# Kernel tuning notes

Hardware: AMD Instinct MI355X
Metric: run time of the kernel (lower is better)

Reference implementation:

```python
import jax, jax.numpy as jnp
from jax import lax
import numpy as np
import math

# --- static config (matches init_kwargs) ---
B, L, C_IN = 64, 1024, 16
D, H, D_FF = 256, 8, 1024
HS, E_LAYERS, OUT = 256, 2, 1
MA, FACTOR = 25, 3
TOP_K = int(FACTOR * math.log(L))  # 20


def _ln(x, g, b, eps=1e-5):
    m = x.mean(-1, keepdims=True)
    v = ((x - m) ** 2).mean(-1, keepdims=True)
    return (x - m) / jnp.sqrt(v + eps) * g + b


def _series_decomp(x, k):
    # x: [B, L, C]; replicate-pad then moving average (AvgPool1d stride 1)
    pad = (k - 1) // 2
    front = jnp.repeat(x[:, :1, :], pad, axis=1)
    end = jnp.repeat(x[:, -1:, :], pad, axis=1)
    xp = jnp.concatenate([front, x, end], axis=1)  # [B, L+k-1, C]
    cs = jnp.cumsum(xp, axis=1)
    cs = jnp.concatenate([jnp.zeros_like(cs[:, :1]), cs], axis=1)
    mm = (cs[:, k:] - cs[:, :-k]) / k  # [B, L, C]
    return x - mm, mm


def _autocorrelation(q, k, v):
    # q,k,v: [B, L, H, E] -> eval-mode Autoformer AutoCorrelation
    Bq, Lq, Hq, Eq = q.shape
    qf = jnp.fft.rfft(q.transpose(0, 2, 3, 1), axis=-1)  # [B,H,E,F]
    kf = jnp.fft.rfft(k.transpose(0, 2, 3, 1), axis=-1)
    corr = jnp.fft.irfft(qf * jnp.conj(kf), n=Lq, axis=-1)  # [B,H,E,L]
    mean_value = corr.mean(axis=(1, 2))  # [B, L]
    weights, delay = lax.top_k(mean_value, TOP_K)  # [B, K]
    tmp_corr = jax.nn.softmax(weights, axis=-1)
    vals = v.transpose(0, 2, 3, 1)  # [B,H,E,L]
    init = jnp.arange(Lq)

    def step(acc, dw):
        d, w = dw  # d: [B] int, w: [B] float
        idx = (init[None, :] + d[:, None]) % Lq  # circular delayed gather == roll
        pat = jnp.take_along_axis(vals, idx[:, None, None, :], axis=-1)
        return acc + pat * w[:, None, None, None], None

    agg, _ = lax.scan(step, jnp.zeros_like(vals), (delay.T, tmp_corr.T))
    return agg.transpose(0, 3, 1, 2)  # [B, L, H, E]


def _forward(x_enc, conv1_w, conv1_b, conv2_w, conv2_b, cnn_ln_g, cnn_ln_b,
             proj_w, proj_b, proj_ln_g, proj_ln_b,
             Wq, bq, Wk, bk, Wv, bv, Wo, bo, Wff1, Wff2,
             rp1_w, rp1_b, rp_ln_g, rp_ln_b, rp2_w, rp2_b):
    Bb = x_enc.shape[0]
    dn = ('NCH', 'OIH', 'NCH')
    # CNN frontend (dropout = identity in eval)
    h = lax.conv_general_dilated(x_enc.transpose(0, 2, 1), conv1_w, (1,), [(1, 1)],
                                 dimension_numbers=dn) + conv1_b[None, :, None]
    h = jax.nn.relu(h)
    h = lax.conv_general_dilated(h, conv2_w, (1,), [(1, 1)],
                                 dimension_numbers=dn) + conv2_b[None, :, None]
    h = jax.nn.relu(h)
    enc = _ln(h.transpose(0, 2, 1), cnn_ln_g, cnn_ln_b)  # [B, L, D]

    pooled_parts = []
    for i in range(E_LAYERS):
        q = (enc @ Wq[i] + bq[i]).reshape(Bb, L, H, D // H)
        k = (enc @ Wk[i] + bk[i]).reshape(Bb, L, H, D // H)
        v = (enc @ Wv[i] + bv[i]).reshape(Bb, L, H, D // H)
        ac = _autocorrelation(q, k, v).reshape(Bb, L, D)
        new_x = ac @ Wo[i] + bo[i]
        x = enc + new_x
        x, _ = _series_decomp(x, MA)
        y = jax.nn.gelu(jnp.einsum('bld,fd->blf', x, Wff1[i]), approximate=False)
        y = jnp.einsum('blf,df->bld', y, Wff2[i])
        enc, _ = _series_decomp(x + y, MA)
        pooled_parts.append(enc[:, -1, :])

    pooled = jnp.concatenate(pooled_parts, axis=-1)  # [B, e_layers*D]
    input_embed = _ln(jax.nn.relu(x_enc.reshape(Bb, -1) @ proj_w + proj_b),
                      proj_ln_g, proj_ln_b)  # [B, HS]
    final = jnp.concatenate([pooled, input_embed], axis=-1)
    o = jax.nn.relu(final @ rp1_w + rp1_b)
    o = _ln(o, rp_ln_g, rp_ln_b)
    o = o @ rp2_w + rp2_b  # [B, 1]
    return o.squeeze(-1)


def setup_inputs() -> dict:
    key = jax.random.key(0)
    ks = iter(jax.random.split(key, 32))

    def nrm(shape, s=0.02):
        return jax.random.normal(next(ks), shape, jnp.float32) * s

    inp = {
        'x_enc': jax.random.normal(next(ks), (B, L, C_IN), jnp.float32),
        'conv1_w': nrm((D, C_IN, 3), 0.1), 'conv1_b': jnp.zeros((D,), jnp.float32),
        'conv2_w': nrm((D, D, 3), 0.05), 'conv2_b': jnp.zeros((D,), jnp.float32),
        'cnn_ln_g': jnp.ones((D,), jnp.float32), 'cnn_ln_b': jnp.zeros((D,), jnp.float32),
        'proj_w': nrm((L * C_IN, HS)), 'proj_b': jnp.zeros((HS,), jnp.float32),
        'proj_ln_g': jnp.ones((HS,), jnp.float32), 'proj_ln_b': jnp.zeros((HS,), jnp.float32),
        'Wq': nrm((E_LAYERS, D, D)), 'bq': jnp.zeros((E_LAYERS, D), jnp.float32),
        'Wk': nrm((E_LAYERS, D, D)), 'bk': jnp.zeros((E_LAYERS, D), jnp.float32),
        'Wv': nrm((E_LAYERS, D, D)), 'bv': jnp.zeros((E_LAYERS, D), jnp.float32),
        'Wo': nrm((E_LAYERS, D, D)), 'bo': jnp.zeros((E_LAYERS, D), jnp.float32),
        'Wff1': nrm((E_LAYERS, D_FF, D)),
        'Wff2': nrm((E_LAYERS, D, D_FF)),
        'rp1_w': nrm((E_LAYERS * D + HS, HS)), 'rp1_b': jnp.zeros((HS,), jnp.float32),
        'rp_ln_g': jnp.ones((HS,), jnp.float32), 'rp_ln_b': jnp.zeros((HS,), jnp.float32),
        'rp2_w': nrm((HS, OUT)), 'rp2_b': jnp.zeros((OUT,), jnp.float32),
    }
    return inp


def reference(x_enc, conv1_w, conv1_b, conv2_w, conv2_b, cnn_ln_g, cnn_ln_b,
              proj_w, proj_b, proj_ln_g, proj_ln_b,
              Wq, bq, Wk, bk, Wv, bv, Wo, bo, Wff1, Wff2,
              rp1_w, rp1_b, rp_ln_g, rp_ln_b, rp2_w, rp2_b):
    return _forward(x_enc, conv1_w, conv1_b, conv2_w, conv2_b, cnn_ln_g, cnn_ln_b,
                    proj_w, proj_b, proj_ln_g, proj_ln_b,
                    Wq, bq, Wk, bk, Wv, bv, Wo, bo, Wff1, Wff2,
                    rp1_w, rp1_b, rp_ln_g, rp_ln_b, rp2_w, rp2_b)
```

## Files before the change

kernel.cpp:

```cpp
#include <hip/hip_runtime.h>
#include <math.h>

#define FLAG_ACC     1
#define FLAG_RELU    2
#define FLAG_GELU    4
#define FLAG_ABF16   8
#define FLAG_OBF16  16
#define FLAG_RESB16 32

typedef __attribute__((ext_vector_type(8))) short short8;
typedef __attribute__((ext_vector_type(4))) short short4v;
typedef __attribute__((ext_vector_type(4))) float f32x4;

__device__ __forceinline__ short f2bf(float f) {
  unsigned u = __builtin_bit_cast(unsigned, f);
  unsigned r = u + 0x7fffu + ((u >> 16) & 1u);
  return (short)(r >> 16);
}
__device__ __forceinline__ float bf2f(short s) {
  unsigned u = ((unsigned)(unsigned short)s) << 16;
  return __builtin_bit_cast(float, u);
}
__device__ __forceinline__ void load_lds16(const void* g, void* lds) {
  __builtin_amdgcn_global_load_lds(
      (const __attribute__((address_space(1))) void*)g,
      (__attribute__((address_space(3))) void*)lds, 16, 0, 0);
}

__global__ __launch_bounds__(256) void gemm_f32(
    const float* __restrict__ A, const float* __restrict__ B, float* __restrict__ C,
    int M, int N, int K, int a_shift,
    const float* __restrict__ bias, const float* __restrict__ residual, int flags)
{
  __shared__ float As[16][65];
  __shared__ float Bs[16][64];
  const int tid = threadIdx.x;
  const int tx = tid & 15, ty = tid >> 4;
  const int row0 = blockIdx.y * 64;
  const int col0 = blockIdx.x * 64;
  int kbeg = 0, kend = K;
  if ((int)gridDim.z > 1) {
    int kchunk = ((K + (int)gridDim.z - 1) / (int)gridDim.z + 15) & ~15;
    kbeg = (int)blockIdx.z * kchunk;
    kend = min(K, kbeg + kchunk);
  }
  float acc[4][4] = {};
  const int a_m = tid >> 2;
  const int a_k = (tid & 3) << 2;
  const int b_n = (tid & 15) << 2;
  const int b_k = tid >> 4;
  for (int k0 = kbeg; k0 < kend; k0 += 16) {
    int srow = row0 + a_m + a_shift;
    float4 av = make_float4(0.f, 0.f, 0.f, 0.f);
    if (srow >= 0 && srow < M)
      av = *reinterpret_cast<const float4*>(A + (long long)srow * K + (k0 + a_k));
    As[a_k + 0][a_m] = av.x; As[a_k + 1][a_m] = av.y;
    As[a_k + 2][a_m] = av.z; As[a_k + 3][a_m] = av.w;
    float4 bv = make_float4(0.f, 0.f, 0.f, 0.f);
    int brow = k0 + b_k;
    if (brow < K)
      bv = *reinterpret_cast<const float4*>(B + (long long)brow * N + (col0 + b_n));
    Bs[b_k][b_n + 0] = bv.x; Bs[b_k][b_n + 1] = bv.y;
    Bs[b_k][b_n + 2] = bv.z; Bs[b_k][b_n + 3] = bv.w;
    __syncthreads();
#pragma unroll
    for (int kk = 0; kk < 16; kk++) {
      float ar[4], br[4];
#pragma unroll
      for (int i = 0; i < 4; i++) ar[i] = As[kk][ty * 4 + i];
#pragma unroll
      for (int j = 0; j < 4; j++) br[j] = Bs[kk][tx * 4 + j];
#pragma unroll
      for (int i = 0; i < 4; i++)
#pragma unroll
        for (int j = 0; j < 4; j++)
          acc[i][j] += ar[i] * br[j];
    }
    __syncthreads();
  }
  if ((int)gridDim.z > 1) {
#pragma unroll
    for (int i = 0; i < 4; i++) {
      int r = row0 + ty * 4 + i; if (r >= M) continue;
#pragma unroll
      for (int j = 0; j < 4; j++) {
        int c = col0 + tx * 4 + j; if (c >= N) continue;
        atomicAdd(&C[(long long)r * N + c], acc[i][j]);
      }
    }
    return;
  }
#pragma unroll
  for (int i = 0; i < 4; i++) {
    int r = row0 + ty * 4 + i; if (r >= M) continue;
#pragma unroll
    for (int j = 0; j < 4; j++) {
      int c = col0 + tx * 4 + j; if (c >= N) continue;
      float v = acc[i][j];
      if (bias)     v += bias[c];
      if (residual) v += residual[(long long)r * N + c];
      if (flags & FLAG_ACC)  v += C[(long long)r * N + c];
      if (flags & FLAG_RELU) v = fmaxf(v, 0.f);
      if (flags & FLAG_GELU) v = 0.5f * v * (1.f + erff(v * 0.70710678118654752f));
      C[(long long)r * N + c] = v;
    }
  }
}

__global__ __launch_bounds__(256) void gemm_bf16_bt(
    const void* __restrict__ Av, const short* __restrict__ Btb, void* __restrict__ Cv,
    const float* __restrict__ residual, const float* __restrict__ bias,
    int M, int N, int K, int lda, int flags, int tapped)
{
  __shared__ __align__(16) short Asl[8192];
  __shared__ __align__(16) short Bsl[8192];
  const int tid = threadIdx.x;
  const int row0 = blockIdx.x * 128;
  const int col0 = blockIdx.y * 128;
  const int lane = tid & 63;
  const int wave = tid >> 6;
  const int wm = (wave >> 1) * 64;
  const int wn = (wave & 1) * 64;
  const int fm = lane & 15;
  const int k8c = lane >> 4;
  const int mr = tid >> 1;
  const int mkc = (tid & 1) * 4;
  const int msw = mr & 7;
  const bool a_dma = (flags & FLAG_ABF16) && !tapped;

  f32x4 acc[4][4] = {};
  for (int k0 = 0; k0 < K; k0 += 64) {
    __syncthreads();
#pragma unroll
    for (int u = 0; u < 4; u++) {
      int p = (wave * 4 + u) * 64 + lane;
      int r = p >> 3;
      int kc = (p & 7) ^ (r & 7);
      load_lds16(Btb + (long long)(col0 + r) * K + k0 + kc * 8,
                 (char*)Bsl + (wave * 4 + u) * 1024);
    }
    if (a_dma) {
      const short* Ab = (const short*)Av;
#pragma unroll
      for (int u = 0; u < 4; u++) {
        int p = (wave * 4 + u) * 64 + lane;
        int r = p >> 3;
        int kc = (p & 7) ^ (r & 7);
        load_lds16(Ab + (long long)(row0 + r) * lda + k0 + kc * 8,
                   (char*)Asl + (wave * 4 + u) * 1024);
      }
    } else {
      int arow = row0 + mr + (tapped ? (k0 >> 8) - 1 : 0);
      int acol = tapped ? (k0 & 255) : k0;
      bool ok = (arow >= 0 && arow < M);
      if (flags & FLAG_ABF16) {
        const short* ga = (const short*)Av + (long long)arow * lda + acol + mkc * 8;
        short8 z;
#pragma unroll
        for (int u = 0; u < 8; u++) z[u] = 0;
#pragma unroll
        for (int j = 0; j < 4; j++) {
          short8 v = ok ? *(const short8*)(ga + j * 8) : z;
          *(short8*)&Asl[(mr * 8 + ((mkc + j) ^ msw)) * 8] = v;
        }
      } else {
        const float* ga = (const float*)Av + (long long)arow * lda + acol + mkc * 8;
#pragma unroll
        for (int j = 0; j < 4; j++) {
          float4 f0 = make_float4(0.f,0.f,0.f,0.f), f1 = f0;
          if (ok) { f0 = *(const float4*)(ga + j * 8); f1 = *(const float4*)(ga + j * 8 + 4); }
          short8 v;
          v[0]=f2bf(f0.x); v[1]=f2bf(f0.y); v[2]=f2bf(f0.z); v[3]=f2bf(f0.w);
          v[4]=f2bf(f1.x); v[5]=f2bf(f1.y); v[6]=f2bf(f1.z); v[7]=f2bf(f1.w);
          *(short8*)&Asl[(mr * 8 + ((mkc + j) ^ msw)) * 8] = v;
        }
      }
    }
    __syncthreads();
#pragma unroll
    for (int kk8 = 0; kk8 < 8; kk8 += 4) {
      short8 af[4], bf[4];
#pragma unroll
      for (int i = 0; i < 4; i++) {
        int r = wm + i * 16 + fm;
        af[i] = *(short8*)&Asl[(r * 8 + ((kk8 + k8c) ^ (r & 7))) * 8];
      }
#pragma unroll
      for (int j = 0; j < 4; j++) {
        int r = wn + j * 16 + fm;
        bf[j] = *(short8*)&Bsl[(r * 8 + ((kk8 + k8c) ^ (r & 7))) * 8];
      }
#pragma unroll
      for (int i = 0; i < 4; i++)
#pragma unroll
        for (int j = 0; j < 4; j++)
          acc[i][j] = __builtin_amdgcn_mfma_f32_16x16x32_bf16(af[i], bf[j], acc[i][j], 0, 0, 0);
    }
  }
#pragma unroll
  for (int i = 0; i < 4; i++) {
    const int mbase = row0 + wm + i * 16 + (lane >> 4) * 4;
#pragma unroll
    for (int j = 0; j < 4; j++) {
      const int n = col0 + wn + j * 16 + fm;
      const float bs = bias ? bias[n] : 0.f;
#pragma unroll
      for (int r = 0; r < 4; r++) {
        long long idx = (long long)(mbase + r) * N + n;
        float v = acc[i][j][r] + bs;
        if (residual) {
          if (flags & FLAG_RESB16) v += bf2f(((const short*)residual)[idx]);
          else                     v += residual[idx];
        }
        if (flags & FLAG_ACC)  v += ((const float*)Cv)[idx];
        if (flags & FLAG_RELU) v = fmaxf(v, 0.f);
        if (flags & FLAG_GELU) v = 0.5f * v * (1.f + erff(v * 0.70710678118654752f));
        if (flags & FLAG_OBF16) ((short*)Cv)[idx] = f2bf(v);
        else                    ((float*)Cv)[idx] = v;
      }
    }
  }
}

__global__ __launch_bounds__(256) void gemm_qk2(
    const short* __restrict__ Ab, const short* __restrict__ Bth,
    const short* __restrict__ Btl,
    short* __restrict__ Ch, short* __restrict__ Cl,
    const float* __restrict__ bias, int M, int N, int K)
{
  __shared__ __align__(16) char smem[24576];
  short* Asl = (short*)smem;
  short* Bhi = (short*)(smem + 8192);
  short* Blo = (short*)(smem + 16384);
  const int tid = threadIdx.x;
  const int row0 = blockIdx.x * 128;
  const int col0 = blockIdx.y * 128;
  const int lane = tid & 63;
  const int wave = tid >> 6;
  const int wm = (wave >> 1) * 64;
  const int wn = (wave & 1) * 64;
  const int fm = lane & 15;
  const int k8c = lane >> 4;

  f32x4 acc[4][4] = {};
  for (int k0 = 0; k0 < K; k0 += 32) {
    __syncthreads();
#pragma unroll
    for (int u = 0; u < 2; u++) {
      int p = (wave + u * 4) * 64 + lane;
      int r = p >> 2;
      int kc = (p & 3) ^ ((r >> 1) & 3);
      long long ao = (long long)(row0 + r) * 256 + k0 + kc * 8;
      long long go = (long long)(col0 + r) * K + k0 + kc * 8;
      int lo = (wave + u * 4) * 1024;
      load_lds16(Ab + ao, (char*)Asl + lo);
      load_lds16(Bth + go, (char*)Bhi + lo);
      load_lds16(Btl + go, (char*)Blo + lo);
    }
    __syncthreads();
    short8 af[4], bh[4], bl[4];
#pragma unroll
    for (int i = 0; i < 4; i++) {
      int r = wm + i * 16 + fm;
      af[i] = *(short8*)&Asl[(r * 4 + (k8c ^ ((r >> 1) & 3))) * 8];
    }
#pragma unroll
    for (int j = 0; j < 4; j++) {
      int r = wn + j * 16 + fm;
      int p = (r * 4 + (k8c ^ ((r >> 1) & 3))) * 8;
      bh[j] = *(short8*)&Bhi[p];
      bl[j] = *(short8*)&Blo[p];
    }
#pragma unroll
    for (int i = 0; i < 4; i++)
#pragma unroll
      for (int j = 0; j < 4; j++) {
        acc[i][j] = __builtin_amdgcn_mfma_f32_16x16x32_bf16(af[i], bh[j], acc[i][j], 0, 0, 0);
        acc[i][j] = __builtin_amdgcn_mfma_f32_16x16x32_bf16(af[i], bl[j], acc[i][j], 0, 0, 0);
      }
  }
#pragma unroll
  for (int i = 0; i < 4; i++) {
    const int mbase = row0 + wm + i * 16 + (lane >> 4) * 4;
#pragma unroll
    for (int j = 0; j < 4; j++) {
      const int n = col0 + wn + j * 16 + fm;
      const float bs = bias ? bias[n] : 0.f;
#pragma unroll
      for (int r = 0; r < 4; r++) {
        long long idx = (long long)(mbase + r) * N + n;
        float v = acc[i][j][r] + bs;
        short h = f2bf(v);
        short l = f2bf(v - bf2f(h));
        Ch[idx] = h; Cl[idx] = l;
      }
    }
  }
}

__global__ __launch_bounds__(256) void corr_mfma3(
    const short* __restrict__ qkh, const short* __restrict__ qkl, float* __restrict__ mv16)
{
  __shared__ __align__(16) char smem[65536];
  short* Ahi = (short*)smem;
  short* Alo = (short*)(smem + 16384);
  short* Bhi = (short*)(smem + 32768);
  short* Blo = (short*)(smem + 49152);
  float* Sf = (float*)smem;

  const int id = blockIdx.x;
  const int b  = (id & 7) + 8 * (id >> 9);
  const int tile = (id >> 3) & 63;
  const int t0 = (tile >> 3) * 128;
  const int s0 = (tile & 7) * 128;
  const int tid = threadIdx.x;
  const int lane = tid & 63;
  const int wave = tid >> 6;
  const int wm = (wave >> 1) * 64;
  const int wn = (wave & 1) * 64;
  const int fm = lane & 15;
  const int k8c = lane >> 4;
  const long long bb = (long long)b * 524288;

  f32x4 acc[4][4] = {};
  for (int k0 = 0; k0 < 256; k0 += 64) {
    __syncthreads();
#pragma unroll
    for (int u = 0; u < 4; u++) {
      int p = (wave * 4 + u) * 64 + lane;
      int r = p >> 3;
      int kc = (p & 7) ^ (r & 7);
      long long qo = bb + (long long)(t0 + r) * 512 + k0 + kc * 8;
      long long ko = bb + (long long)(s0 + r) * 512 + 256 + k0 + kc * 8;
      int lo = (wave * 4 + u) * 1024;
      load_lds16(qkh + qo, (char*)Ahi + lo);
      load_lds16(qkl + qo, (char*)Alo + lo);
      load_lds16(qkh + ko, (char*)Bhi + lo);
      load_lds16(qkl + ko, (char*)Blo + lo);
    }
    __syncthreads();
#pragma unroll
    for (int kk8 = 0; kk8 < 8; kk8 += 4) {
      short8 ah[4], al[4], bh[4], bl[4];
#pragma unroll
      for (int i = 0; i < 4; i++) {
        int r = wm + i * 16 + fm;
        int p = (r * 8 + ((kk8 + k8c) ^ (r & 7))) * 8;
        ah[i] = *(short8*)&Ahi[p];
        al[i] = *(short8*)&Alo[p];
      }
#pragma unroll
      for (int j = 0; j < 4; j++) {
        int r = wn + j * 16 + fm;
        int p = (r * 8 + ((kk8 + k8c) ^ (r & 7))) * 8;
        bh[j] = *(short8*)&Bhi[p];
        bl[j] = *(short8*)&Blo[p];
      }
#pragma unroll
      for (int i = 0; i < 4; i++)
#pragma unroll
        for (int j = 0; j < 4; j++) {
          acc[i][j] = __builtin_amdgcn_mfma_f32_16x16x32_bf16(ah[i], bh[j], acc[i][j], 0, 0, 0);
          acc[i][j] = __builtin_amdgcn_mfma_f32_16x16x32_bf16(ah[i], bl[j], acc[i][j], 0, 0, 0);
          acc[i][j] = __builtin_amdgcn_mfma_f32_16x16x32_bf16(al[i], bh[j], acc[i][j], 0, 0, 0);
        }
    }
  }
  __syncthreads();
#pragma unroll
  for (int i = 0; i < 4; i++) {
    const int row = wm + i * 16 + (lane >> 4) * 4;
#pragma unroll
    for (int j = 0; j < 4; j++) {
      const int col = wn + j * 16 + fm;
#pragma unroll
      for (int r = 0; r < 4; r++)
        Sf[(row + r) * 128 + ((2 * (row + r) - col) & 127)] =
            acc[i][j][r] * (1.f / 256.f);
    }
  }
  __syncthreads();
  {
    const int dd = tid & 127;
    const int mb = (tid >> 7) * 64;
    float s_ge = 0.f, s_lt = 0.f;
    for (int mm = 0; mm < 64; mm++) {
      int m = mb + mm;
      float v = Sf[m * 128 + ((dd + m) & 127)];
      if (m >= dd) s_ge += v; else s_lt += v;
    }
    __syncthreads();
    Sf[tid] = s_ge;
    Sf[256 + tid] = s_lt;
    __syncthreads();
    if (tid < 128) {
      float ge = Sf[tid] + Sf[tid + 128];
      float lt = Sf[256 + tid] + Sf[256 + tid + 128];
      const int sl = t0 >> 7;
      mv16[((long long)sl * 64 + b) * 1024 + ((t0 - s0 + tid) & 1023)] = ge;
      mv16[((long long)(8 + sl) * 64 + b) * 1024 + ((t0 - s0 + tid - 128) & 1023)] = lt;
    }
  }
}

__global__ void prep_weights(
    const float* __restrict__ conv2_w, const float* __restrict__ Wq,
    const float* __restrict__ Wk, const float* __restrict__ Wff1,
    const float* __restrict__ Wff2,
    const float* __restrict__ bq, const float* __restrict__ bk,
    short* __restrict__ CB2Tb, short* __restrict__ QKTH, short* __restrict__ QKTL,
    short* __restrict__ WFF1b, short* __restrict__ WFF2b, float* __restrict__ BQK)
{
  const int total = 196608 + 262144 + 524288 + 524288 + 1024;
  for (int idx = blockIdx.x * 256 + threadIdx.x; idx < total;
       idx += gridDim.x * 256) {
    int t = idx;
    if (t < 196608) {
      int o = t / 768, rem = t % 768, kk = rem >> 8, i = rem & 255;
      CB2Tb[t] = f2bf(conv2_w[(o * 256 + i) * 3 + kk]);
    } else if ((t -= 196608) < 262144) {
      int L = t >> 17, rem = t & 131071, r = rem >> 8, k = rem & 255;
      float val = (r < 256) ? Wq[L * 65536 + k * 256 + r]
                            : Wk[L * 65536 + k * 256 + (r - 256)];
      short h = f2bf(val);
      QKTH[t] = h;
      QKTL[t] = f2bf(val - bf2f(h));
    } else if ((t -= 262144) < 524288) {
      WFF1b[t] = f2bf(Wff1[t]);
    } else if ((t -= 524288) < 524288) {
      WFF2b[t] = f2bf(Wff2[t]);
    } else {
      t -= 524288;
      int L = t >> 9, j = t & 511;
      BQK[t] = (j < 256) ? bq[L * 256 + j] : bk[L * 256 + (j - 256)];
    }
  }
}

__global__ void vo_finish(const float* __restrict__ WVO, const float* __restrict__ Wo,
                          const float* __restrict__ bv, const float* __restrict__ bo,
                          short* __restrict__ WVOTb, float* __restrict__ BVO)
{
  const int total = 131072 + 512;
  for (int idx = blockIdx.x * 256 + threadIdx.x; idx < total;
       idx += gridDim.x * 256) {
    if (idx < 131072) {
      int L = idx >> 16, rem = idx & 65535, n = rem >> 8, k = rem & 255;
      WVOTb[idx] = f2bf(WVO[L * 65536 + k * 256 + n]);
    } else {
      int j = idx - 131072;
      int L = j >> 8, n = j & 255;
      float acc = bo[L * 256 + n];
      for (int k = 0; k < 256; k++)
        acc += bv[L * 256 + k] * Wo[(long long)L * 65536 + k * 256 + n];
      BVO[j] = acc;
    }
  }
}

__global__ __launch_bounds__(256) void conv1_direct(
    const float* __restrict__ x, const float* __restrict__ w,
    const float* __restrict__ bias, short* __restrict__ out)
{
  __shared__ float xs[66][16];
  const int b = blockIdx.y, lg = blockIdx.x, tid = threadIdx.x;
  const int l0 = lg * 64;
  for (int idx = tid; idx < 1056; idx += 256) {
    int r = idx >> 4, c = idx & 15;
    int l = l0 + r - 1;
    xs[r][c] = (l >= 0 && l < 1024) ? x[((long long)b * 1024 + l) * 16 + c] : 0.f;
  }
  float wr[48];
#pragma unroll
  for (int u = 0; u < 48; u++) wr[u] = w[tid * 48 + u];
  const float bs = bias[tid];
  __syncthreads();
  for (int r = 0; r < 64; r++) {
    float acc = bs;
#pragma unroll
    for (int i = 0; i < 16; i++) {
      acc += xs[r + 0][i] * wr[i * 3 + 0];
      acc += xs[r + 1][i] * wr[i * 3 + 1];
      acc += xs[r + 2][i] * wr[i * 3 + 2];
    }
    out[((long long)b * 1024 + l0 + r) * 256 + tid] = f2bf(fmaxf(acc, 0.f));
  }
}

__global__ void fixup_conv_b(short* __restrict__ h, const short* __restrict__ src,
                             const float* __restrict__ w, const float* __restrict__ bias)
{
  int b = blockIdx.x >> 1;
  int l = (blockIdx.x & 1) ? 1023 : 0;
  int o = threadIdx.x;
  float acc = bias[o];
  for (int kk = 0; kk < 3; kk++) {
    int t = l + kk - 1;
    if (t < 0 || t > 1023) continue;
    const short* srow = src + ((long long)b * 1024 + t) * 256;
    const float* wrow = w + (long long)o * 256 * 3 + kk;
    for (int i = 0; i < 256; i++) acc += bf2f(srow[i]) * wrow[(long long)i * 3];
  }
  h[((long long)b * 1024 + l) * 256 + o] = f2bf(fmaxf(acc, 0.f));
}

__global__ __launch_bounds__(256) void ln_rows4(
    const float* __restrict__ in, float* __restrict__ out,
    const float* __restrict__ g, const float* __restrict__ b,
    int prerelu, int out_stride, int out_off)
{
  const int row = blockIdx.x * 4 + (threadIdx.x >> 6);
  const int lane = threadIdx.x & 63;
  float4 x = ((const float4*)(in + (long long)row * 256))[lane];
  if (prerelu) {
    x.x = fmaxf(x.x, 0.f); x.y = fmaxf(x.y, 0.f);
    x.z = fmaxf(x.z, 0.f); x.w = fmaxf(x.w, 0.f);
  }
  float s = x.x + x.y + x.z + x.w;
#pragma unroll
  for (int o = 32; o > 0; o >>= 1) s += __shfl_xor(s, o, 64);
  float mean = s * (1.f / 256.f);
  float4 d = make_float4(x.x - mean, x.y - mean, x.z - mean, x.w - mean);
  float s2 = d.x * d.x + d.y * d.y + d.z * d.z + d.w * d.w;
#pragma unroll
  for (int o = 32; o > 0; o >>= 1) s2 += __shfl_xor(s2, o, 64);
  float rsd = rsqrtf(s2 * (1.f / 256.f) + 1e-5f);
  float4 gg = ((const float4*)g)[lane];
  float4 bb = ((const float4*)b)[lane];
  float4 o4 = make_float4(d.x * rsd * gg.x + bb.x, d.y * rsd * gg.y + bb.y,
                          d.z * rsd * gg.z + bb.z, d.w * rsd * gg.w + bb.w);
  ((float4*)(out + (long long)row * out_stride + out_off))[lane] = o4;
}

__global__ __launch_bounds__(256) void ln_rows4bb(
    const short* __restrict__ in, short* __restrict__ out,
    const float* __restrict__ g, const float* __restrict__ b)
{
  const int row = blockIdx.x * 4 + (threadIdx.x >> 6);
  const int lane = threadIdx.x & 63;
  short4v xb = ((const short4v*)in)[(long long)row * 64 + lane];
  float4 x = make_float4(bf2f(xb[0]), bf2f(xb[1]), bf2f(xb[2]), bf2f(xb[3]));
  float s = x.x + x.y + x.z + x.w;
#pragma unroll
  for (int o = 32; o > 0; o >>= 1) s += __shfl_xor(s, o, 64);
  float mean = s * (1.f / 256.f);
  float4 d = make_float4(x.x - mean, x.y - mean, x.z - mean, x.w - mean);
  float s2 = d.x * d.x + d.y * d.y + d.z * d.z + d.w * d.w;
#pragma unroll
  for (int o = 32; o > 0; o >>= 1) s2 += __shfl_xor(s2, o, 64);
  float rsd = rsqrtf(s2 * (1.f / 256.f) + 1e-5f);
  float4 gg = ((const float4*)g)[lane];
  float4 bb = ((const float4*)b)[lane];
  short4v o4;
  o4[0] = f2bf(d.x * rsd * gg.x + bb.x);
  o4[1] = f2bf(d.y * rsd * gg.y + bb.y);
  o4[2] = f2bf(d.z * rsd * gg.z + bb.z);
  o4[3] = f2bf(d.w * rsd * gg.w + bb.w);
  ((short4v*)out)[(long long)row * 64 + lane] = o4;
}

__global__ void decomp4bf(const short* __restrict__ in, short* __restrict__ out,
                          float* __restrict__ fin, int finoff)
{
  const int id = blockIdx.x;
  const int c = id & 7;
  const int s = id >> 3;
  const int b = c + 8 * (s >> 8);
  const int lg = s & 255;
  const int l = lg * 4 + (threadIdx.x >> 6);
  const int c4 = threadIdx.x & 63;
  const short4v* base = (const short4v*)(in + (long long)b * 262144);
  float4 acc = make_float4(0.f, 0.f, 0.f, 0.f);
#pragma unroll
  for (int j = -12; j <= 12; j++) {
    int t = l + j;
    t = t < 0 ? 0 : (t > 1023 ? 1023 : t);
    short4v x = base[t * 64 + c4];
    acc.x += bf2f(x[0]); acc.y += bf2f(x[1]);
    acc.z += bf2f(x[2]); acc.w += bf2f(x[3]);
  }
  short4v x0 = base[l * 64 + c4];
  float4 o = make_float4(bf2f(x0[0]) - acc.x * (1.f / 25.f),
                         bf2f(x0[1]) - acc.y * (1.f / 25.f),
                         bf2f(x0[2]) - acc.z * (1.f / 25.f),
                         bf2f(x0[3]) - acc.w * (1.f / 25.f));
  short4v ob;
  ob[0] = f2bf(o.x); ob[1] = f2bf(o.y); ob[2] = f2bf(o.z); ob[3] = f2bf(o.w);
  ((short4v*)out)[((long long)b * 1024 + l) * 64 + c4] = ob;
  if (l == 1023) {
    float* f = fin + (long long)b * 768 + finoff + c4 * 4;
    f[0] = o.x; f[1] = o.y; f[2] = o.z; f[3] = o.w;
  }
}

__global__ void decomp4b(const short* __restrict__ in, short* __restrict__ out)
{
  const int id = blockIdx.x;
  const int c = id & 7;
  const int s = id >> 3;
  const int b = c + 8 * (s >> 8);
  const int lg = s & 255;
  const int l = lg * 4 + (threadIdx.x >> 6);
  const int c4 = threadIdx.x & 63;
  const short4v* base = (const short4v*)(in + (long long)b * 262144);
  float4 acc = make_float4(0.f, 0.f, 0.f, 0.f);
#pragma unroll
  for (int j = -12; j <= 12; j++) {
    int t = l + j;
    t = t < 0 ? 0 : (t > 1023 ? 1023 : t);
    short4v x = base[t * 64 + c4];
    acc.x += bf2f(x[0]); acc.y += bf2f(x[1]);
    acc.z += bf2f(x[2]); acc.w += bf2f(x[3]);
  }
  short4v x0 = base[l * 64 + c4];
  short4v o;
  o[0] = f2bf(bf2f(x0[0]) - acc.x * (1.f / 25.f));
  o[1] = f2bf(bf2f(x0[1]) - acc.y * (1.f / 25.f));
  o[2] = f2bf(bf2f(x0[2]) - acc.z * (1.f / 25.f));
  o[3] = f2bf(bf2f(x0[3]) - acc.w * (1.f / 25.f));
  ((short4v*)(out + (long long)b * 262144))[l * 64 + c4] = o;
}

__global__ __launch_bounds__(64) void topk_softmax_wave(
    const float* __restrict__ mv16, float* __restrict__ wts, int* __restrict__ dly)
{
  const int b = blockIdx.x, lane = threadIdx.x;
  float v[16];
#pragma unroll
  for (int j = 0; j < 16; j++) {
    float s = 0.f;
#pragma unroll
    for (int sl = 0; sl < 16; sl++)
      s += mv16[((long long)sl * 64 + b) * 1024 + lane + 64 * j];
    v[j] = s;
  }
  float selv = 0.f; int seli = 0;
  for (int it = 0; it < 20; it++) {
    float bv = -1e30f; int bi = 0x7fffffff;
#pragma unroll
    for (int j = 0; j < 16; j++) {
      float x = v[j]; int idx = lane + 64 * j;
      if (x > bv || (x == bv && idx < bi)) { bv = x; bi = idx; }
    }
#pragma unroll
    for (int off = 32; off > 0; off >>= 1) {
      float ov = __shfl_xor(bv, off, 64);
      int   oi = __shfl_xor(bi, off, 64);
      if (ov > bv || (ov == bv && oi < bi)) { bv = ov; bi = oi; }
    }
    if (lane == it) { selv = bv; seli = bi; }
    if ((bi & 63) == lane) v[bi >> 6] = -1e30f;
  }
  const float w0 = __shfl(selv, 0, 64);
  float e = (lane < 20) ? __expf(selv - w0) : 0.f;
  float s = e;
#pragma unroll
  for (int off = 32; off > 0; off >>= 1) s += __shfl_xor(s, off, 64);
  if (lane < 20) {
    wts[b * 20 + lane] = e / s;
    dly[b * 20 + lane] = seli;
  }
}

__global__ void agg4b(const short* __restrict__ enc, const float* __restrict__ wts,
                      const int* __restrict__ dly, short* __restrict__ out)
{
  const int id = blockIdx.x;
  const int c = id & 7;
  const int s = id >> 3;
  const int b = c + 8 * (s >> 8);
  const int lg = s & 255;
  const int l = lg * 4 + (threadIdx.x >> 6);
  const int c4 = threadIdx.x & 63;
  const short4v* vb = (const short4v*)(enc + (long long)b * 262144);
  float4 acc = make_float4(0.f, 0.f, 0.f, 0.f);
  for (int kk = 0; kk < 20; kk++) {
    int d = dly[b * 20 + kk];
    float w = wts[b * 20 + kk];
    short4v x = vb[((l + d) & 1023) * 64 + c4];
    acc.x += w * bf2f(x[0]); acc.y += w * bf2f(x[1]);
    acc.z += w * bf2f(x[2]); acc.w += w * bf2f(x[3]);
  }
  short4v o;
  o[0] = f2bf(acc.x); o[1] = f2bf(acc.y); o[2] = f2bf(acc.z); o[3] = f2bf(acc.w);
  ((short4v*)(out + (long long)b * 262144))[l * 64 + c4] = o;
}

__global__ void init_bias(float* __restrict__ C, const float* __restrict__ bias)
{
  C[(long long)blockIdx.x * 256 + threadIdx.x] = bias[threadIdx.x];
}

__global__ void rp2_kernel(const float* __restrict__ x, const float* __restrict__ w,
                           const float* __restrict__ bias, float* __restrict__ out)
{
  __shared__ float red[4];
  int b = blockIdx.x, tid = threadIdx.x;
  float p = x[b * 256 + tid] * w[tid];
#pragma unroll
  for (int o = 32; o > 0; o >>= 1) p += __shfl_down(p, o, 64);
  if ((tid & 63) == 0) red[tid >> 6] = p;
  __syncthreads();
  if (tid == 0) out[b] = red[0] + red[1] + red[2] + red[3] + bias[0];
}

static inline void gemm(hipStream_t s, const float* A, const float* B, float* C,
                        int M, int N, int K, int shift, const float* bias,
                        const float* res, int flags, int splitz = 1)
{
  dim3 g((N + 63) / 64, (M + 63) / 64, splitz);
  gemm_f32<<<g, dim3(256), 0, s>>>(A, B, C, M, N, K, shift, bias, res, flags);
}

extern "C" void kernel_launch(void* const* d_in, const int* in_sizes, int n_in,
                              void* d_out, int out_size, void* d_ws, size_t ws_size,
                              hipStream_t stream)
{
  const float* x_enc  = (const float*)d_in[0];
  const float* conv1_w= (const float*)d_in[1];
  const float* conv1_b= (const float*)d_in[2];
  const float* conv2_w= (const float*)d_in[3];
  const float* conv2_b= (const float*)d_in[4];
  const float* cnn_g  = (const float*)d_in[5];
  const float* cnn_b  = (const float*)d_in[6];
  const float* proj_w = (const float*)d_in[7];
  const float* proj_b = (const float*)d_in[8];
  const float* pln_g  = (const float*)d_in[9];
  const float* pln_b  = (const float*)d_in[10];
  const float* Wq     = (const float*)d_in[11];
  const float* bq     = (const float*)d_in[12];
  const float* Wk     = (const float*)d_in[13];
  const float* bk     = (const float*)d_in[14];
  const float* Wv     = (const float*)d_in[15];
  const float* bv     = (const float*)d_in[16];
  const float* Wo     = (const float*)d_in[17];
  const float* bo     = (const float*)d_in[18];
  const float* Wff1   = (const float*)d_in[19];
  const float* Wff2   = (const float*)d_in[20];
  const float* rp1_w  = (const float*)d_in[21];
  const float* rp1_b  = (const float*)d_in[22];
  const float* rln_g  = (const float*)d_in[23];
  const float* rln_b  = (const float*)d_in[24];
  const float* rp2_w  = (const float*)d_in[25];
  const float* rp2_b  = (const float*)d_in[26];
  (void)in_sizes; (void)n_in;

  const size_t BLD = 64ull * 1024 * 256;
  size_t need;
  {
    size_t o = 3 * BLD
             + 98304 + 131072 + 131072 + 262144 + 262144
             + 65536 + 512 + 1024
             + 1048576 + 1280 + 1280 + 16384 + 49152 + 16384 + 16384;
    need = o * sizeof(float);
  }
  if (ws_size < need) {
    hipMemsetAsync(d_out, 0, (size_t)out_size * sizeof(float), stream);
    return;
  }

  float* ws = (float*)d_ws;
  size_t off = 0;
  auto alloc = [&](size_t n) { float* p = ws + off; off += n; return p; };
  float* BUF0 = alloc(BLD);
  float* BUF1 = alloc(BLD);
  float* BUF2 = alloc(BLD);
  short* CB2Tb = (short*)alloc(98304);
  short* QKTH  = (short*)alloc(131072);
  short* QKTL  = (short*)alloc(131072);
  short* WFF1b = (short*)alloc(262144);
  short* WFF2b = (short*)alloc(262144);
  short* WVOTb = (short*)alloc(65536);
  float* BVO  = alloc(512);
  float* BQK  = alloc(1024);
  float* MV16 = alloc(1048576);
  float* WTS  = alloc(1280);
  int*   DLY  = (int*)alloc(1280);
  float* PE   = alloc(16384);
  float* FIN  = alloc(49152);
  float* O1   = alloc(16384);
  float* O2   = alloc(16384);
  float* WVO  = BUF0;
  short* ENC  = (short*)BUF2;

  const int M = 65536;
  dim3 blk(256);

  prep_weights<<<1024, blk, 0, stream>>>(conv2_w, Wq, Wk, Wff1, Wff2, bq, bk,
                                         CB2Tb, QKTH, QKTL, WFF1b, WFF2b, BQK);
  for (int i = 0; i < 2; i++)
    gemm(stream, Wv + (size_t)i * 65536, Wo + (size_t)i * 65536,
         WVO + (size_t)i * 65536, 256, 256, 256, 0, nullptr, nullptr, 0);
  vo_finish<<<516, blk, 0, stream>>>(WVO, Wo, bv, bo, WVOTb, BVO);

  conv1_direct<<<dim3(16, 64), blk, 0, stream>>>(x_enc, conv1_w, conv1_b, (short*)BUF0);
  gemm_bf16_bt<<<dim3(512, 2), blk, 0, stream>>>(
      BUF0, CB2Tb, BUF1, nullptr, conv2_b, M, 256, 768, 256,
      FLAG_ABF16 | FLAG_RELU | FLAG_OBF16, 1);
  fixup_conv_b<<<128, blk, 0, stream>>>((short*)BUF1, (const short*)BUF0,
                                        conv2_w, conv2_b);
  ln_rows4bb<<<16384, blk, 0, stream>>>((const short*)BUF1, ENC, cnn_g, cnn_b);

  for (int i = 0; i < 2; i++) {
    short* QKH = (short*)BUF0;
    short* QKL = (short*)BUF1;
    gemm_qk2<<<dim3(512, 4), blk, 0, stream>>>(
        ENC, QKTH + (size_t)i * 131072, QKTL + (size_t)i * 131072,
        QKH, QKL, BQK + i * 512, M, 512, 256);
    corr_mfma3<<<dim3(4096), blk, 0, stream>>>(QKH, QKL, MV16);
    topk_softmax_wave<<<64, dim3(64), 0, stream>>>(MV16, WTS, DLY);
    agg4b<<<dim3(16384), blk, 0, stream>>>(ENC, WTS, DLY, (short*)BUF0);
    gemm_bf16_bt<<<dim3(512, 2), blk, 0, stream>>>(
        BUF0, WVOTb + (size_t)i * 65536, BUF1, (const float*)ENC, BVO + i * 256,
        M, 256, 256, 256, FLAG_ABF16 | FLAG_OBF16 | FLAG_RESB16, 0);
    decomp4b<<<16384, blk, 0, stream>>>((const short*)BUF1, (short*)BUF0);
    for (int c = 0; c < 2; c++) {
      const short* xd = (const short*)BUF0 + (size_t)c * 32768 * 256;
      gemm_bf16_bt<<<dim3(256, 8), blk, 0, stream>>>(
          xd, WFF1b + (size_t)i * 262144, BUF2, nullptr, nullptr,
          32768, 1024, 256, 256, FLAG_ABF16 | FLAG_GELU | FLAG_OBF16, 0);
      gemm_bf16_bt<<<dim3(256, 2), blk, 0, stream>>>(
          BUF2, WFF2b + (size_t)i * 262144,
          (short*)BUF1 + (size_t)c * 32768 * 256,
          (const float*)xd, nullptr,
          32768, 256, 1024, 1024, FLAG_ABF16 | FLAG_RESB16 | FLAG_OBF16, 0);
    }
    decomp4bf<<<16384, blk, 0, stream>>>((const short*)BUF1, ENC, FIN, i * 256);
  }

  init_bias<<<64, blk, 0, stream>>>(PE, proj_b);
  gemm(stream, x_enc, proj_w, PE, 64, 256, 16384, 0, nullptr, nullptr, 0, 32);
  ln_rows4<<<16, blk, 0, stream>>>(PE, FIN, pln_g, pln_b, 1, 768, 512);
  init_bias<<<64, blk, 0, stream>>>(O1, rp1_b);
  gemm(stream, FIN, rp1_w, O1, 64, 256, 768, 0, nullptr, nullptr, 0, 4);
  ln_rows4<<<16, blk, 0, stream>>>(O1, O2, rln_g, rln_b, 1, 256, 0);
  rp2_kernel<<<64, blk, 0, stream>>>(O2, rp2_w, rp2_b, (float*)d_out);
}
```

Before: 1.517 ms.

## Replace MFMA cross-correlation with FFT-based correlation over transposed Q/K

The Q/K projection GEMM now writes fp32 output transposed per batch and channel instead of split-bf16 hi/lo rows. The direct time-domain cross-correlation (3-pass bf16 MFMA over all lag pairs) is replaced by a radix-4 shared-memory FFT that packs Q and K into one complex transform, accumulates Q·conj(K) spectra over channel groups, and does one inverse FFT per batch. This cuts the O(L^2·D) correlation work to O(L log L·D) and removes the 16-slice mean reduction in top-k. The trade-off is low parallelism in the inverse kernel (64 blocks), many barriers per FFT, and a switch to fp32 FFT rounding instead of split-bf16 products.

```diff
diff --git a/kernel.cpp b/kernel.cpp
--- a/kernel.cpp
+++ b/kernel.cpp
@@ -222,11 +222,10 @@
   }
 }
 
-__global__ __launch_bounds__(256) void gemm_qk2(
+__global__ __launch_bounds__(256) void gemm_qkT(
     const short* __restrict__ Ab, const short* __restrict__ Bth,
-    const short* __restrict__ Btl,
-    short* __restrict__ Ch, short* __restrict__ Cl,
-    const float* __restrict__ bias, int M, int N, int K)
+    const short* __restrict__ Btl, float* __restrict__ QT,
+    const float* __restrict__ bias, int K)
 {
   __shared__ __align__(16) char smem[24576];
   short* Asl = (short*)smem;
@@ -282,124 +281,144 @@
 #pragma unroll
   for (int i = 0; i < 4; i++) {
     const int mbase = row0 + wm + i * 16 + (lane >> 4) * 4;
+    const int bb = mbase >> 10;
+    const int l  = mbase & 1023;
 #pragma unroll
     for (int j = 0; j < 4; j++) {
       const int n = col0 + wn + j * 16 + fm;
-      const float bs = bias ? bias[n] : 0.f;
-#pragma unroll
-      for (int r = 0; r < 4; r++) {
-        long long idx = (long long)(mbase + r) * N + n;
-        float v = acc[i][j][r] + bs;
-        short h = f2bf(v);
-        short l = f2bf(v - bf2f(h));
-        Ch[idx] = h; Cl[idx] = l;
-      }
-    }
-  }
-}
-
-__global__ __launch_bounds__(256) void corr_mfma3(
-    const short* __restrict__ qkh, const short* __restrict__ qkl, float* __restrict__ mv16)
-{
-  __shared__ __align__(16) char smem[65536];
-  short* Ahi = (short*)smem;
-  short* Alo = (short*)(smem + 16384);
-  short* Bhi = (short*)(smem + 32768);
-  short* Blo = (short*)(smem + 49152);
-  float* Sf = (float*)smem;
-
-  const int id = blockIdx.x;
-  const int b  = (id & 7) + 8 * (id >> 9);
-  const int tile = (id >> 3) & 63;
-  const int t0 = (tile >> 3) * 128;
-  const int s0 = (tile & 7) * 128;
+      const float bs = bias[n];
+      float4 o = make_float4(acc[i][j][0] + bs, acc[i][j][1] + bs,
+                             acc[i][j][2] + bs, acc[i][j][3] + bs);
+      *(float4*)&QT[((long long)(bb * 512 + n) << 10) + l] = o;
+    }
+  }
+}
+
+#define SKW(i) ((i) + ((i) >> 5))
+
+__device__ __forceinline__ int rev4_10(int f) {
+  return ((f & 3) << 8) | (((f >> 2) & 3) << 6) | (((f >> 4) & 3) << 4)
+       | (((f >> 6) & 3) << 2) | ((f >> 8) & 3);
+}
+
+template<int M, bool INV>
+__device__ __forceinline__ void fft_stage(const float2* __restrict__ s,
+                                          float2* __restrict__ d,
+                                          const float2* __restrict__ tw, int t) {
+  constexpr int LOG2M = (M == 256) ? 8 : (M == 64) ? 6 : (M == 16) ? 4 : (M == 4) ? 2 : 0;
+  const int j = t & (M - 1);
+  const int base = ((t >> LOG2M) << (LOG2M + 2)) | j;
+  float2 a = s[SKW(base)];
+  float2 b = s[SKW(base + M)];
+  float2 c = s[SKW(base + 2 * M)];
+  float2 e = s[SKW(base + 3 * M)];
+  float t0r = a.x + c.x, t0i = a.y + c.y;
+  float t1r = a.x - c.x, t1i = a.y - c.y;
+  float t2r = b.x + e.x, t2i = b.y + e.y;
+  float t3r = b.x - e.x, t3i = b.y - e.y;
+  float y0r = t0r + t2r, y0i = t0i + t2i;
+  float y2r = t0r - t2r, y2i = t0i - t2i;
+  float y1r, y1i, y3r, y3i;
+  if (!INV) { y1r = t1r + t3i; y1i = t1i - t3r; y3r = t1r - t3i; y3i = t1i + t3r; }
+  else      { y1r = t1r - t3i; y1i = t1i + t3r; y3r = t1r + t3i; y3i = t1i - t3r; }
+  float2 w = tw[SKW(j << (8 - LOG2M))];
+  float c1 = w.x, s1 = INV ? -w.y : w.y;
+  float c2 = c1 * c1 - s1 * s1, s2 = 2.f * c1 * s1;
+  float c3 = c2 * c1 - s2 * s1, s3 = c2 * s1 + s2 * c1;
+  d[SKW(base)]         = make_float2(y0r, y0i);
+  d[SKW(base + M)]     = make_float2(y1r * c1 - y1i * s1, y1r * s1 + y1i * c1);
+  d[SKW(base + 2 * M)] = make_float2(y2r * c2 - y2i * s2, y2r * s2 + y2i * c2);
+  d[SKW(base + 3 * M)] = make_float2(y3r * c3 - y3i * s3, y3r * s3 + y3i * c3);
+}
+
+__global__ __launch_bounds__(256) void fft_cross(
+    const float* __restrict__ QT, float* __restrict__ Rpart)
+{
+  __shared__ float2 ping[1056], pong[1056], tw[264];
   const int tid = threadIdx.x;
-  const int lane = tid & 63;
-  const int wave = tid >> 6;
-  const int wm = (wave >> 1) * 64;
-  const int wn = (wave & 1) * 64;
-  const int fm = lane & 15;
-  const int k8c = lane >> 4;
-  const long long bb = (long long)b * 524288;
-
-  f32x4 acc[4][4] = {};
-  for (int k0 = 0; k0 < 256; k0 += 64) {
+  const int b = blockIdx.x & 63;
+  const int g = blockIdx.x >> 6;
+  {
+    float s, c;
+    sincosf(-1.5707963267948966f * (float)tid * (1.f / 256.f), &s, &c);
+    tw[SKW(tid)] = make_float2(c, s);
+  }
+  const float* Qb = QT + (long long)b * 524288;
+  const int c0 = g * 32;
+  float4 qv = *(const float4*)(Qb + ((long long)c0 << 10) + tid * 4);
+  float4 kv = *(const float4*)(Qb + ((long long)(256 + c0) << 10) + tid * 4);
+  float aR[4] = {0.f, 0.f, 0.f, 0.f}, aI[4] = {0.f, 0.f, 0.f, 0.f};
+  __syncthreads();
+  for (int cc = 0; cc < 32; cc++) {
+    const int i0 = tid * 4;
+    ping[SKW(i0 + 0)] = make_float2(qv.x, kv.x);
+    ping[SKW(i0 + 1)] = make_float2(qv.y, kv.y);
+    ping[SKW(i0 + 2)] = make_float2(qv.z, kv.z);
+    ping[SKW(i0 + 3)] = make_float2(qv.w, kv.w);
+    if (cc < 31) {
+      int c = c0 + cc + 1;
+      qv = *(const float4*)(Qb + ((long long)c << 10) + tid * 4);
+      kv = *(const float4*)(Qb + ((long long)(256 + c) << 10) + tid * 4);
+    }
     __syncthreads();
+    fft_stage<256, false>(ping, pong, tw, tid); __syncthreads();
+    fft_stage<64,  false>(pong, ping, tw, tid); __syncthreads();
+    fft_stage<16,  false>(ping, pong, tw, tid); __syncthreads();
+    fft_stage<4,   false>(pong, ping, tw, tid); __syncthreads();
+    fft_stage<1,   false>(ping, pong, tw, tid); __syncthreads();
 #pragma unroll
     for (int u = 0; u < 4; u++) {
-      int p = (wave * 4 + u) * 64 + lane;
-      int r = p >> 3;
-      int kc = (p & 7) ^ (r & 7);
-      long long qo = bb + (long long)(t0 + r) * 512 + k0 + kc * 8;
-      long long ko = bb + (long long)(s0 + r) * 512 + 256 + k0 + kc * 8;
-      int lo = (wave * 4 + u) * 1024;
-      load_lds16(qkh + qo, (char*)Ahi + lo);
-      load_lds16(qkl + qo, (char*)Alo + lo);
-      load_lds16(qkh + ko, (char*)Bhi + lo);
-      load_lds16(qkl + ko, (char*)Blo + lo);
-    }
-    __syncthreads();
-#pragma unroll
-    for (int kk8 = 0; kk8 < 8; kk8 += 4) {
-      short8 ah[4], al[4], bh[4], bl[4];
-#pragma unroll
-      for (int i = 0; i < 4; i++) {
-        int r = wm + i * 16 + fm;
-        int p = (r * 8 + ((kk8 + k8c) ^ (r & 7))) * 8;
-        ah[i] = *(short8*)&Ahi[p];
-        al[i] = *(short8*)&Alo[p];
-      }
-#pragma unroll
-      for (int j = 0; j < 4; j++) {
-        int r = wn + j * 16 + fm;
-        int p = (r * 8 + ((kk8 + k8c) ^ (r & 7))) * 8;
-        bh[j] = *(short8*)&Bhi[p];
-        bl[j] = *(short8*)&Blo[p];
-      }
-#pragma unroll
-      for (int i = 0; i < 4; i++)
-#pragma unroll
-        for (int j = 0; j < 4; j++) {
-          acc[i][j] = __builtin_amdgcn_mfma_f32_16x16x32_bf16(ah[i], bh[j], acc[i][j], 0, 0, 0);
-          acc[i][j] = __builtin_amdgcn_mfma_f32_16x16x32_bf16(ah[i], bl[j], acc[i][j], 0, 0, 0);
-          acc[i][j] = __builtin_amdgcn_mfma_f32_16x16x32_bf16(al[i], bh[j], acc[i][j], 0, 0, 0);
-        }
-    }
+      int f = tid + (u << 8);
+      float2 z1 = pong[SKW(rev4_10(f))];
+      float2 z2 = pong[SKW(rev4_10((1024 - f) & 1023))];
+      float Qr = 0.5f * (z1.x + z2.x), Qi = 0.5f * (z1.y - z2.y);
+      float Kr = 0.5f * (z1.y + z2.y), Ki = 0.5f * (z2.x - z1.x);
+      aR[u] += Qr * Kr + Qi * Ki;
+      aI[u] += Qi * Kr - Qr * Ki;
+    }
+  }
+  float* Rp = Rpart + (long long)(g * 64 + b) * 2048;
+#pragma unroll
+  for (int u = 0; u < 4; u++) {
+    Rp[tid + (u << 8)] = aR[u];
+    Rp[1024 + tid + (u << 8)] = aI[u];
+  }
+}
+
+__global__ __launch_bounds__(256) void fft_inv(
+    const float* __restrict__ Rpart, float* __restrict__ MV)
+{
+  __shared__ float2 ping[1056], pong[1056], tw[264];
+  const int tid = threadIdx.x;
+  const int b = blockIdx.x;
+  {
+    float s, c;
+    sincosf(-1.5707963267948966f * (float)tid * (1.f / 256.f), &s, &c);
+    tw[SKW(tid)] = make_float2(c, s);
+  }
+#pragma unroll
+  for (int u = 0; u < 4; u++) {
+    int f = tid + (u << 8);
+    float sr = 0.f, si = 0.f;
+#pragma unroll
+    for (int g = 0; g < 8; g++) {
+      const float* Rp = Rpart + (long long)(g * 64 + b) * 2048;
+      sr += Rp[f];
+      si += Rp[1024 + f];
+    }
+    ping[SKW(f)] = make_float2(sr, si);
   }
   __syncthreads();
-#pragma unroll
-  for (int i = 0; i < 4; i++) {
-    const int row = wm + i * 16 + (lane >> 4) * 4;
-#pragma unroll
-    for (int j = 0; j < 4; j++) {
-      const int col = wn + j * 16 + fm;
-#pragma unroll
-      for (int r = 0; r < 4; r++)
-        Sf[(row + r) * 128 + ((2 * (row + r) - col) & 127)] =
-            acc[i][j][r] * (1.f / 256.f);
-    }
-  }
-  __syncthreads();
-  {
-    const int dd = tid & 127;
-    const int mb = (tid >> 7) * 64;
-    float s_ge = 0.f, s_lt = 0.f;
-    for (int mm = 0; mm < 64; mm++) {
-      int m = mb + mm;
-      float v = Sf[m * 128 + ((dd + m) & 127)];
-      if (m >= dd) s_ge += v; else s_lt += v;
-    }
-    __syncthreads();
-    Sf[tid] = s_ge;
-    Sf[256 + tid] = s_lt;
-    __syncthreads();
-    if (tid < 128) {
-      float ge = Sf[tid] + Sf[tid + 128];
-      float lt = Sf[256 + tid] + Sf[256 + tid + 128];
-      const int sl = t0 >> 7;
-      mv16[((long long)sl * 64 + b) * 1024 + ((t0 - s0 + tid) & 1023)] = ge;
-      mv16[((long long)(8 + sl) * 64 + b) * 1024 + ((t0 - s0 + tid - 128) & 1023)] = lt;
-    }
+  fft_stage<256, true>(ping, pong, tw, tid); __syncthreads();
+  fft_stage<64,  true>(pong, ping, tw, tid); __syncthreads();
+  fft_stage<16,  true>(ping, pong, tw, tid); __syncthreads();
+  fft_stage<4,   true>(pong, ping, tw, tid); __syncthreads();
+  fft_stage<1,   true>(ping, pong, tw, tid); __syncthreads();
+  const float sc = 1.f / (1024.f * 256.f);
+#pragma unroll
+  for (int u = 0; u < 4; u++) {
+    int p = tid + (u << 8);
+    MV[(long long)b * 1024 + rev4_10(p)] = pong[SKW(p)].x * sc;
   }
 }
 
@@ -622,18 +641,13 @@
 }
 
 __global__ __launch_bounds__(64) void topk_softmax_wave(
-    const float* __restrict__ mv16, float* __restrict__ wts, int* __restrict__ dly)
+    const float* __restrict__ mv, float* __restrict__ wts, int* __restrict__ dly)
 {
   const int b = blockIdx.x, lane = threadIdx.x;
   float v[16];
 #pragma unroll
-  for (int j = 0; j < 16; j++) {
-    float s = 0.f;
-#pragma unroll
-    for (int sl = 0; sl < 16; sl++)
-      s += mv16[((long long)sl * 64 + b) * 1024 + lane + 64 * j];
-    v[j] = s;
-  }
+  for (int j = 0; j < 16; j++)
+    v[j] = mv[(long long)b * 1024 + lane + 64 * j];
   float selv = 0.f; int seli = 0;
   for (int it = 0; it < 20; it++) {
     float bv = -1e30f; int bi = 0x7fffffff;
@@ -782,6 +796,8 @@
   float* O2   = alloc(16384);
   float* WVO  = BUF0;
   short* ENC  = (short*)BUF2;
+  float* QT   = BUF0;
+  float* MV   = BUF2 + 8388608;
 
   const int M = 65536;
   dim3 blk(256);
@@ -802,13 +818,12 @@
   ln_rows4bb<<<16384, blk, 0, stream>>>((const short*)BUF1, ENC, cnn_g, cnn_b);
 
   for (int i = 0; i < 2; i++) {
-    short* QKH = (short*)BUF0;
-    short* QKL = (short*)BUF1;
-    gemm_qk2<<<dim3(512, 4), blk, 0, stream>>>(
+    gemm_qkT<<<dim3(512, 4), blk, 0, stream>>>(
         ENC, QKTH + (size_t)i * 131072, QKTL + (size_t)i * 131072,
-        QKH, QKL, BQK + i * 512, M, 512, 256);
-    corr_mfma3<<<dim3(4096), blk, 0, stream>>>(QKH, QKL, MV16);
-    topk_softmax_wave<<<64, dim3(64), 0, stream>>>(MV16, WTS, DLY);
+        QT, BQK + i * 512, 256);
+    fft_cross<<<512, blk, 0, stream>>>(QT, MV16);
+    fft_inv<<<64, blk, 0, stream>>>(MV16, MV);
+    topk_softmax_wave<<<64, dim3(64), 0, stream>>>(MV, WTS, DLY);
     agg4b<<<dim3(16384), blk, 0, stream>>>(ENC, WTS, DLY, (short*)BUF0);
     gemm_bf16_bt<<<dim3(512, 2), blk, 0, stream>>>(
         BUF0, WVOTb + (size_t)i * 65536, BUF1, (const float*)ENC, BVO + i * 256,
```

Result: no change. 1.494 ms (-1.5%).
